# Kernel tuning notes

Hardware: AMD Instinct MI355X
Metric: run time of the kernel (lower is better)

Reference implementation:

```python
import jax, jax.numpy as jnp
import numpy as np

D = 1024        # input_dim
H = 4096        # hidden_dim (expert FFN width)
RH = H // 2     # router hidden
E = 8           # expert_count
TOP_K = 2
N = 4096        # tokens
LN_EPS = 1e-5


def setup_inputs() -> dict:
    key = jax.random.key(0)
    ks = jax.random.split(key, 12)
    s_d = 1.0 / np.sqrt(D)
    s_h = 1.0 / np.sqrt(H)
    s_rh = 1.0 / np.sqrt(RH)
    return {
        "x": jax.random.normal(ks[0], (N, D), jnp.float32),
        "ln_g": jnp.ones((D,), jnp.float32),
        "ln_b": jnp.zeros((D,), jnp.float32),
        # router: Linear(D, RH) -> ReLU -> Linear(RH, E)
        "rw1": jax.random.uniform(ks[1], (D, RH), jnp.float32, -s_d, s_d),
        "rb1": jax.random.uniform(ks[2], (RH,), jnp.float32, -s_d, s_d),
        "rw2": jax.random.uniform(ks[3], (RH, E), jnp.float32, -s_rh, s_rh),
        "rb2": jax.random.uniform(ks[4], (E,), jnp.float32, -s_rh, s_rh),
        # experts: E x (Linear(D, H) -> ReLU -> Linear(H, D)); dropout is identity in eval
        "ew1": jax.random.uniform(ks[5], (E, D, H), jnp.float32, -s_d, s_d),
        "eb1": jax.random.uniform(ks[6], (E, H), jnp.float32, -s_d, s_d),
        "ew2": jax.random.uniform(ks[7], (E, H, D), jnp.float32, -s_h, s_h),
        "eb2": jax.random.uniform(ks[8], (E, D), jnp.float32, -s_h, s_h),
    }


def reference(x, ln_g, ln_b, rw1, rb1, rw2, rb2, ew1, eb1, ew2, eb2):
    residual = x
    # LayerNorm
    mu = jnp.mean(x, axis=-1, keepdims=True)
    var = jnp.mean(jnp.square(x - mu), axis=-1, keepdims=True)
    xn = (x - mu) * jax.lax.rsqrt(var + LN_EPS) * ln_g + ln_b
    # Router MLP + softmax + top-k with renormalized gates
    logits = jax.nn.relu(xn @ rw1 + rb1) @ rw2 + rb2          # [N, E]
    probs = jax.nn.softmax(logits, axis=-1)
    vals, idx = jax.lax.top_k(probs, TOP_K)                    # [N, K]
    vals = vals / jnp.sum(vals, axis=-1, keepdims=True)
    # combine weights per expert: [N, E]
    combine = jnp.sum(jax.nn.one_hot(idx, E, dtype=vals.dtype) * vals[..., None], axis=1)
    # dense grouped expert FFN: h [E, N, H], y [E, N, D]
    h = jax.nn.relu(jnp.einsum("nd,edh->enh", xn, ew1) + eb1[:, None, :])
    y = jnp.einsum("enh,ehd->end", h, ew2) + eb2[:, None, :]
    out = residual + jnp.einsum("end,ne->nd", y, combine)
    return out
```

## Files before the change

kernel.cpp:

```cpp
#include <hip/hip_runtime.h>
#include <stdint.h>

#define D_    1024
#define H_    4096
#define RH_   2048
#define E_    8
#define N_    4096
#define NK_   8192
#define MT_MAX 71
#define DELTA_MARGIN 1e-4f
#define FIX_CAP 256

typedef __bf16 bf16x8 __attribute__((ext_vector_type(8)));
typedef float  f32x4  __attribute__((ext_vector_type(4)));


__device__ __forceinline__ unsigned short f2bf(float f) {
  union { float f; unsigned u; } v; v.f = f;
  unsigned r = v.u + 0x7fffu + ((v.u >> 16) & 1u);
  return (unsigned short)(r >> 16);
}
__device__ __forceinline__ float bf2f(unsigned short h) {
  union { unsigned u; float f; } v; v.u = ((unsigned)h) << 16;
  return v.f;
}

#define GLOAD16(gp, lp) \
  __builtin_amdgcn_global_load_lds((__attribute__((address_space(1))) void*)(void*)(gp), \
                                   (__attribute__((address_space(3))) void*)(lp), 16, 0, 0)

__global__ __launch_bounds__(256) void k_transpose(const float* __restrict__ in,
                                                   unsigned short* __restrict__ outH,
                                                   unsigned short* __restrict__ outL,
                                                   int R, int C) {
  __shared__ float t[64][65];
  const int b = blockIdx.z;
  const int c0 = blockIdx.x * 64, r0 = blockIdx.y * 64;
  const int lx = threadIdx.x & 63, ly = threadIdx.x >> 6;
  const long inB = (long)R * C;
  const float* ip = in + b * inB + (long)r0 * C + c0 + lx;
  #pragma unroll
  for (int i = 0; i < 16; i++)
    t[ly + i * 4][lx] = ip[(long)(ly + i * 4) * C];
  __syncthreads();
  const int wy = threadIdx.x >> 2;
  const int wx = (threadIdx.x & 3) * 16;
  const int c = c0 + wy;
  const long ob = b * inB + (long)c * R + r0 + wx;
  unsigned short h[16];
  #pragma unroll
  for (int j = 0; j < 16; j++) h[j] = f2bf(t[wx + j][wy]);
  #pragma unroll
  for (int j = 0; j < 4; j++)
    *(ushort4*)&outH[ob + j * 4] = make_ushort4(h[j*4], h[j*4+1], h[j*4+2], h[j*4+3]);
  if (outL) {
    unsigned short l[16];
    #pragma unroll
    for (int j = 0; j < 16; j++) l[j] = f2bf(t[wx + j][wy] - bf2f(h[j]));
    #pragma unroll
    for (int j = 0; j < 4; j++)
      *(ushort4*)&outL[ob + j * 4] = make_ushort4(l[j*4], l[j*4+1], l[j*4+2], l[j*4+3]);
  }
}

__global__ __launch_bounds__(256) void k_layernorm(const float* __restrict__ x,
                                                   const float* __restrict__ g,
                                                   const float* __restrict__ b,
                                                   unsigned short* __restrict__ xnh,
                                                   unsigned short* __restrict__ xnl) {
  __shared__ float red[4];
  const int n = blockIdx.x, tid = threadIdx.x;
  float4 v = ((const float4*)(x + (long)n * D_))[tid];
  float s = v.x + v.y + v.z + v.w;
  #pragma unroll
  for (int o = 32; o >= 1; o >>= 1) s += __shfl_xor(s, o, 64);
  if ((tid & 63) == 0) red[tid >> 6] = s;
  __syncthreads();
  float mean = (red[0] + red[1] + red[2] + red[3]) * (1.f / D_);
  __syncthreads();
  float d0 = v.x - mean, d1 = v.y - mean, d2 = v.z - mean, d3 = v.w - mean;
  float ss = d0 * d0 + d1 * d1 + d2 * d2 + d3 * d3;
  #pragma unroll
  for (int o = 32; o >= 1; o >>= 1) ss += __shfl_xor(ss, o, 64);
  if ((tid & 63) == 0) red[tid >> 6] = ss;
  __syncthreads();
  float rstd = rsqrtf((red[0] + red[1] + red[2] + red[3]) * (1.f / D_) + 1e-5f);
  float4 gg = ((const float4*)g)[tid];
  float4 bb = ((const float4*)b)[tid];
  float xn0 = d0 * rstd * gg.x + bb.x;
  float xn1 = d1 * rstd * gg.y + bb.y;
  float xn2 = d2 * rstd * gg.z + bb.z;
  float xn3 = d3 * rstd * gg.w + bb.w;
  unsigned short h0 = f2bf(xn0), h1 = f2bf(xn1), h2 = f2bf(xn2), h3 = f2bf(xn3);
  ((ushort4*)xnh)[(long)n * 256 + tid] = make_ushort4(h0, h1, h2, h3);
  ((ushort4*)xnl)[(long)n * 256 + tid] = make_ushort4(
      f2bf(xn0 - bf2f(h0)), f2bf(xn1 - bf2f(h1)),
      f2bf(xn2 - bf2f(h2)), f2bf(xn3 - bf2f(h3)));
}

__global__ void k_init(int* ctl) { if (threadIdx.x < 36) ctl[threadIdx.x] = 0; }

__global__ __launch_bounds__(256) void k_router_gemm(const unsigned short* __restrict__ xh,
                                                     const unsigned short* __restrict__ xl,
                                                     const unsigned short* __restrict__ bhT,
                                                     const unsigned short* __restrict__ blT,
                                                     const float* __restrict__ rb1,
                                                     float* __restrict__ h_r) {
  __shared__ __align__(16) unsigned short Ah[128 * 32], Al[128 * 32], Bh[128 * 32], Bl[128 * 32];
  const int tid = threadIdx.x, lane = tid & 63, wid = tid >> 6;
  const int m0 = blockIdx.x * 128, n0 = blockIdx.y * 128;
  const int wm = wid >> 1, wn = wid & 1;
  const int seg0 = wid * 2;
  const int srow = lane >> 2;
  const int scol = (lane & 3) * 8;
  const long a0 = (long)(m0 + seg0 * 16 + srow) * D_ + scol;
  const long a1 = a0 + 16 * D_;
  const long b0 = (long)(n0 + seg0 * 16 + srow) * D_ + scol;
  const long b1 = b0 + 16 * D_;
  const int rl = lane & 15, kh8 = (lane >> 4) * 8;
  f32x4 acc[4][4];
  #pragma unroll
  for (int i = 0; i < 4; i++)
    #pragma unroll
    for (int j = 0; j < 4; j++) acc[i][j] = 0.f;

  for (int k0 = 0; k0 < D_; k0 += 32) {
    GLOAD16(xh + a0 + k0, Ah + seg0 * 512);
    GLOAD16(xh + a1 + k0, Ah + seg0 * 512 + 512);
    GLOAD16(xl + a0 + k0, Al + seg0 * 512);
    GLOAD16(xl + a1 + k0, Al + seg0 * 512 + 512);
    GLOAD16(bhT + b0 + k0, Bh + seg0 * 512);
    GLOAD16(bhT + b1 + k0, Bh + seg0 * 512 + 512);
    GLOAD16(blT + b0 + k0, Bl + seg0 * 512);
    GLOAD16(blT + b1 + k0, Bl + seg0 * 512 + 512);
    __syncthreads();
    bf16x8 bhf[4], blf[4];
    #pragma unroll
    for (int ni = 0; ni < 4; ni++) {
      int r = (wn * 64 + ni * 16 + rl) * 32 + kh8;
      bhf[ni] = *(const bf16x8*)(Bh + r);
      blf[ni] = *(const bf16x8*)(Bl + r);
    }
    #pragma unroll
    for (int mi = 0; mi < 4; mi++) {
      int r = (wm * 64 + mi * 16 + rl) * 32 + kh8;
      bf16x8 ah = *(const bf16x8*)(Ah + r);
      bf16x8 al = *(const bf16x8*)(Al + r);
      #pragma unroll
      for (int ni = 0; ni < 4; ni++) {
        acc[mi][ni] = __builtin_amdgcn_mfma_f32_16x16x32_bf16(ah, bhf[ni], acc[mi][ni], 0, 0, 0);
        acc[mi][ni] = __builtin_amdgcn_mfma_f32_16x16x32_bf16(ah, blf[ni], acc[mi][ni], 0, 0, 0);
        acc[mi][ni] = __builtin_amdgcn_mfma_f32_16x16x32_bf16(al, bhf[ni], acc[mi][ni], 0, 0, 0);
      }
    }
    __syncthreads();
  }
  const int rg4 = (lane >> 4) * 4;
  #pragma unroll
  for (int ni = 0; ni < 4; ni++) {
    int col = n0 + wn * 64 + ni * 16 + rl;
    float bias = rb1[col];
    #pragma unroll
    for (int mi = 0; mi < 4; mi++) {
      int row = m0 + wm * 64 + mi * 16 + rg4;
      #pragma unroll
      for (int r = 0; r < 4; r++) {
        float v = acc[mi][ni][r] + bias;
        h_r[(long)(row + r) * RH_ + col] = v > 0.f ? v : 0.f;
      }
    }
  }
}

__global__ __launch_bounds__(256) void k_logits_top2(const float* __restrict__ h_r,
                                                     const float* __restrict__ rw2,
                                                     const float* __restrict__ rb2,
                                                     int* __restrict__ sel, float* __restrict__ gate,
                                                     int* __restrict__ marked, int* __restrict__ mcount) {
  const int lane = threadIdx.x & 63, wid = threadIdx.x >> 6;
  const int n = blockIdx.x * 4 + wid;
  float p[8] = {0, 0, 0, 0, 0, 0, 0, 0};
  const float* hr = h_r + (long)n * RH_;
  for (int i = 0; i < RH_ / 64; i++) {
    int c = i * 64 + lane;
    float v = hr[c];
    float4 wa = ((const float4*)(rw2 + c * 8))[0];
    float4 wb = ((const float4*)(rw2 + c * 8))[1];
    p[0] += v * wa.x; p[1] += v * wa.y; p[2] += v * wa.z; p[3] += v * wa.w;
    p[4] += v * wb.x; p[5] += v * wb.y; p[6] += v * wb.z; p[7] += v * wb.w;
  }
  #pragma unroll
  for (int e = 0; e < 8; e++)
    #pragma unroll
    for (int s = 32; s >= 1; s >>= 1) p[e] += __shfl_xor(p[e], s, 64);
  if (lane == 0) {
    float l1 = -1e30f, l2 = -1e30f, l3 = -1e30f; int e1 = 0, e2 = 0;
    #pragma unroll
    for (int e = 0; e < 8; e++) {
      float v = p[e] + rb2[e];
      if (v > l1)      { l3 = l2; l2 = l1; e2 = e1; l1 = v; e1 = e; }
      else if (v > l2) { l3 = l2; l2 = v; e2 = e; }
      else if (v > l3) { l3 = v; }
    }
    float g1 = 1.f / (1.f + expf(l2 - l1));
    sel[n * 2] = e1; sel[n * 2 + 1] = e2;
    gate[n * 2] = g1; gate[n * 2 + 1] = 1.f - g1;
    if (l2 - l3 < DELTA_MARGIN) { int i = atomicAdd(mcount, 1); marked[i] = n; }
  }
}

__global__ __launch_bounds__(256) void k_fixup1(const float* __restrict__ x,
                                                const float* __restrict__ ln_g, const float* __restrict__ ln_b,
                                                const float* __restrict__ rw1, const float* __restrict__ rb1,
                                                const int* __restrict__ marked, const int* __restrict__ mcount,
                                                double* __restrict__ hsbuf) {
  __shared__ float xs[D_];
  __shared__ float redf[4];
  __shared__ double part[64][5];
  const int tid = threadIdx.x;
  int cnt = *mcount; if (cnt > FIX_CAP) cnt = FIX_CAP;
  const int blkTok = blockIdx.x >> 5;
  const int chunk  = blockIdx.x & 31;
  for (int mi = blkTok; mi < cnt; mi += FIX_CAP) {
    const int n = marked[mi];
    float4 v = ((const float4*)(x + (long)n * D_))[tid];
    float s = v.x + v.y + v.z + v.w;
    #pragma unroll
    for (int o = 32; o >= 1; o >>= 1) s += __shfl_xor(s, o, 64);
    if ((tid & 63) == 0) redf[tid >> 6] = s;
    __syncthreads();
    float mean = (redf[0] + redf[1] + redf[2] + redf[3]) * (1.f / D_);
    __syncthreads();
    float d0 = v.x - mean, d1 = v.y - mean, d2 = v.z - mean, d3 = v.w - mean;
    float ss = d0 * d0 + d1 * d1 + d2 * d2 + d3 * d3;
    #pragma unroll
    for (int o = 32; o >= 1; o >>= 1) ss += __shfl_xor(ss, o, 64);
    if ((tid & 63) == 0) redf[tid >> 6] = ss;
    __syncthreads();
    float rstd = rsqrtf((redf[0] + redf[1] + redf[2] + redf[3]) * (1.f / D_) + 1e-5f);
    float4 gg = ((const float4*)ln_g)[tid];
    float4 bb = ((const float4*)ln_b)[tid];
    xs[tid * 4 + 0] = d0 * rstd * gg.x + bb.x;
    xs[tid * 4 + 1] = d1 * rstd * gg.y + bb.y;
    xs[tid * 4 + 2] = d2 * rstd * gg.z + bb.z;
    xs[tid * 4 + 3] = d3 * rstd * gg.w + bb.w;
    __syncthreads();
    const int lcol = tid & 63, prt = tid >> 6;
    const int col = chunk * 64 + lcol;
    const float* rp = rw1 + (long)(prt * 256) * RH_ + col;
    const float* xp = xs + prt * 256;
    double a0 = 0, a1 = 0, a2 = 0, a3 = 0;
    #pragma unroll 4
    for (int d = 0; d < 256; d += 4) {
      float w0 = rp[(long)(d + 0) * RH_];
      float w1 = rp[(long)(d + 1) * RH_];
      float w2 = rp[(long)(d + 2) * RH_];
      float w3 = rp[(long)(d + 3) * RH_];
      a0 += (double)xp[d + 0] * (double)w0;
      a1 += (double)xp[d + 1] * (double)w1;
      a2 += (double)xp[d + 2] * (double)w2;
      a3 += (double)xp[d + 3] * (double)w3;
    }
    part[lcol][prt] = (a0 + a1) + (a2 + a3);
    __syncthreads();
    if (tid < 64) {
      double a = (part[tid][0] + part[tid][1]) + (part[tid][2] + part[tid][3])
               + (double)rb1[chunk * 64 + tid];
      hsbuf[(long)mi * RH_ + chunk * 64 + tid] = a > 0.0 ? a : 0.0;
    }
    __syncthreads();
  }
}

__global__ __launch_bounds__(256) void k_fixup2(const double* __restrict__ hsbuf,
                                                const float* __restrict__ rw2, const float* __restrict__ rb2,
                                                const int* __restrict__ marked, const int* __restrict__ mcount,
                                                int* __restrict__ sel, float* __restrict__ gate) {
  __shared__ double red2[256];
  const int tid = threadIdx.x;
  int cnt = *mcount; if (cnt > FIX_CAP) cnt = FIX_CAP;
  for (int mi = blockIdx.x; mi < cnt; mi += gridDim.x) {
    const int n = marked[mi];
    const double* hs = hsbuf + (long)mi * RH_;
    const int e = tid & 7, ch = tid >> 3;
    double pp = 0.0;
    for (int c = ch * 64; c < ch * 64 + 64; c++) pp += hs[c] * (double)rw2[c * 8 + e];
    red2[tid] = pp;
    __syncthreads();
    if (tid < 128) red2[tid] += red2[tid + 128];
    __syncthreads();
    if (tid < 64) red2[tid] += red2[tid + 64];
    __syncthreads();
    if (tid < 32) red2[tid] += red2[tid + 32];
    __syncthreads();
    if (tid < 16) red2[tid] += red2[tid + 16];
    __syncthreads();
    if (tid < 8) red2[tid] += red2[tid + 8];
    __syncthreads();
    if (tid == 0) {
      double l1 = -1e300, l2 = -1e300; int e1 = 0, e2 = 0;
      for (int ee = 0; ee < 8; ee++) {
        double vv = red2[ee] + (double)rb2[ee];
        if (vv > l1)      { l2 = l1; e2 = e1; l1 = vv; e1 = ee; }
        else if (vv > l2) { l2 = vv; e2 = ee; }
      }
      double g1 = 1.0 / (1.0 + exp(l2 - l1));
      sel[n * 2] = e1; sel[n * 2 + 1] = e2;
      gate[n * 2] = (float)g1; gate[n * 2 + 1] = (float)(1.0 - g1);
    }
    __syncthreads();
  }
}

__global__ void k_count(const int* __restrict__ sel, int* ctl) {
  int n = blockIdx.x * 256 + threadIdx.x;
  if (n >= N_) return;
  atomicAdd(&ctl[sel[n * 2]], 1);
  atomicAdd(&ctl[sel[n * 2 + 1]], 1);
}
__global__ void k_offsets(int* ctl) {
  if (threadIdx.x == 0 && blockIdx.x == 0) {
    int t = 0, tt = 0;
    for (int e = 0; e < 8; e++) {
      ctl[8 + e] = t; ctl[17 + e] = tt; ctl[26 + e] = t;
      t += ctl[e]; tt += (ctl[e] + 127) >> 7;
    }
    ctl[16] = t; ctl[25] = tt;
  }
}
__global__ void k_scatter(const int* __restrict__ sel, int* ctl,
                          int* __restrict__ perm, int* __restrict__ pos) {
  int n = blockIdx.x * 256 + threadIdx.x;
  if (n >= N_) return;
  #pragma unroll
  for (int k = 0; k < 2; k++) {
    int e = sel[n * 2 + k];
    int p = atomicAdd(&ctl[26 + e], 1);
    perm[p] = n;
    pos[n * 2 + k] = p;
  }
}

template <int KD, bool GATHER, bool RELU_BF16, bool MTFAST>
__global__ __launch_bounds__(256) void k_gemm_expert5(const unsigned short* __restrict__ A,
                                                      const unsigned short* __restrict__ BT,
                                                      const float* __restrict__ bias,
                                                      const int* __restrict__ ctl,
                                                      const int* __restrict__ perm,
                                                      unsigned short* __restrict__ outBF,
                                                      float* __restrict__ outF32, int NB) {
  const int* cnt = ctl; const int* off = ctl + 8; const int* toff = ctl + 17;
  const int NX = gridDim.x, MT = gridDim.y;
  const int nwg = NX * MT;
  const int F = blockIdx.y * NX + blockIdx.x;
  const int q = nwg >> 3, r8 = nwg & 7;
  const int xcd = F & 7, j = F >> 3;
  const int L = (xcd < r8 ? xcd * (q + 1) : r8 * (q + 1) + (xcd - r8) * q) + j;
  int mt, nt;
  if (MTFAST) { mt = L % MT; nt = L / MT; }
  else        { nt = L % NX; mt = L / NX; }
  if (mt >= toff[8]) return;
  int e = 0;
  #pragma unroll
  for (int i = 0; i < 7; i++) if (toff[i + 1] <= mt) e = i + 1;
  const int ltile = mt - toff[e];
  const int g0 = off[e] + ltile * 128;
  int vrows = cnt[e] - ltile * 128; if (vrows > 128) vrows = 128;
  const int n0 = nt * 128;

  __shared__ __align__(16) unsigned short At[2][128 * 64];
  __shared__ __align__(16) unsigned short Bt[2][128 * 64];
  const int tid = threadIdx.x, lane = tid & 63, wid = tid >> 6;
  const int l8 = lane >> 3, s8 = lane & 7;
  const int ksw = (s8 ^ l8) * 8;

  long aa[4], bb[4];
  const long bbase = (long)e * NB * KD;
  const int gmax = off[e] + cnt[e] - 1;
  #pragma unroll
  for (int i = 0; i < 4; i++) {
    int row = wid * 32 + i * 8 + l8;
    long ar;
    if constexpr (GATHER) {
      int g = g0 + row;
      ar = perm[g <= gmax ? g : gmax];
    } else {
      ar = g0 + row;
    }
    aa[i] = ar * (long)KD + ksw;
    bb[i] = bbase + (long)(n0 + row) * KD + ksw;
  }

  const int wm = wid >> 1, wn = wid & 1;
  const int rl = lane & 15, g4 = lane >> 4;
  int sA[2];
  #pragma unroll
  for (int kk = 0; kk < 2; kk++)
    sA[kk] = ((kk * 4 + g4) ^ (rl & 7)) * 8;

  f32x4 acc[4][4];
  #pragma unroll
  for (int i = 0; i < 4; i++)
    #pragma unroll
    for (int jj = 0; jj < 4; jj++) acc[i][jj] = 0.f;

  auto stage = [&](int bi, int k0) {
    #pragma unroll
    for (int i = 0; i < 4; i++) {
      GLOAD16(A + aa[i] + k0, &At[bi][(wid * 32 + i * 8) * 64]);
      GLOAD16(BT + bb[i] + k0, &Bt[bi][(wid * 32 + i * 8) * 64]);
    }
  };
  auto compute = [&](int bi) {
    #pragma unroll
    for (int kk = 0; kk < 2; kk++) {
      bf16x8 bfr[4];
      #pragma unroll
      for (int ni = 0; ni < 4; ni++)
        bfr[ni] = *(const bf16x8*)(&Bt[bi][(wn * 64 + ni * 16 + rl) * 64 + sA[kk]]);
      #pragma unroll
      for (int mi = 0; mi < 4; mi++) {
        bf16x8 af = *(const bf16x8*)(&At[bi][(wm * 64 + mi * 16 + rl) * 64 + sA[kk]]);
        #pragma unroll
        for (int ni = 0; ni < 4; ni++)
          acc[mi][ni] = __builtin_amdgcn_mfma_f32_16x16x32_bf16(af, bfr[ni], acc[mi][ni], 0, 0, 0);
      }
    }
  };

  constexpr int NT = KD / 64;
  stage(0, 0);
  stage(1, 64);
  int cur = 0;
  #pragma unroll 1
  for (int t = 0; t < NT - 2; ++t) {
    asm volatile("s_waitcnt vmcnt(8)" ::: "memory");
    __builtin_amdgcn_sched_barrier(0);
    __builtin_amdgcn_s_barrier();
    asm volatile("" ::: "memory");
    compute(cur);
    asm volatile("" ::: "memory");
    __builtin_amdgcn_s_barrier();
    stage(cur, (t + 2) * 64);
    cur ^= 1;
  }
  asm volatile("s_waitcnt vmcnt(8)" ::: "memory");
  __builtin_amdgcn_sched_barrier(0);
  __builtin_amdgcn_s_barrier();
  asm volatile("" ::: "memory");
  compute(cur);
  asm volatile("" ::: "memory");
  __builtin_amdgcn_s_barrier();
  cur ^= 1;
  asm volatile("s_waitcnt vmcnt(0)" ::: "memory");
  __builtin_amdgcn_sched_barrier(0);
  __builtin_amdgcn_s_barrier();
  asm volatile("" ::: "memory");
  compute(cur);

  const int rg4 = (lane >> 4) * 4;
  #pragma unroll
  for (int ni = 0; ni < 4; ni++) {
    int col = n0 + wn * 64 + ni * 16 + rl;
    float bv = bias[(long)e * NB + col];
    #pragma unroll
    for (int mi = 0; mi < 4; mi++) {
      int lrow = wm * 64 + mi * 16 + rg4;
      #pragma unroll
      for (int r = 0; r < 4; r++) {
        if (lrow + r < vrows) {
          float v = acc[mi][ni][r] + bv;
          long idx = (long)(g0 + lrow + r) * NB + col;
          if constexpr (RELU_BF16) outBF[idx] = f2bf(v > 0.f ? v : 0.f);
          else outF32[idx] = v;
        }
      }
    }
  }
}

__global__ __launch_bounds__(256) void k_combine(const float* __restrict__ x,
                                                 const float* __restrict__ y_buf,
                                                 const int* __restrict__ pos,
                                                 const float* __restrict__ gate,
                                                 float* __restrict__ out) {
  const int n = blockIdx.x, t = threadIdx.x;
  const float g0 = gate[n * 2], g1 = gate[n * 2 + 1];
  const long p0 = pos[n * 2], p1 = pos[n * 2 + 1];
  float4 xv = ((const float4*)(x + (long)n * D_))[t];
  float4 a = ((const float4*)(y_buf + p0 * D_))[t];
  float4 b = ((const float4*)(y_buf + p1 * D_))[t];
  float4 o;
  o.x = xv.x + g0 * a.x + g1 * b.x;
  o.y = xv.y + g0 * a.y + g1 * b.y;
  o.z = xv.z + g0 * a.z + g1 * b.z;
  o.w = xv.w + g0 * a.w + g1 * b.w;
  ((float4*)(out + (long)n * D_))[t] = o;
}

extern "C" void kernel_launch(void* const* d_in, const int* in_sizes, int n_in,
                              void* d_out, int out_size, void* d_ws, size_t ws_size,
                              hipStream_t stream) {
  const float* x    = (const float*)d_in[0];
  const float* ln_g = (const float*)d_in[1];
  const float* ln_b = (const float*)d_in[2];
  const float* rw1  = (const float*)d_in[3];
  const float* rb1  = (const float*)d_in[4];
  const float* rw2  = (const float*)d_in[5];
  const float* rb2  = (const float*)d_in[6];
  const float* ew1  = (const float*)d_in[7];
  const float* eb1  = (const float*)d_in[8];
  const float* ew2  = (const float*)d_in[9];
  const float* eb2  = (const float*)d_in[10];
  float* out = (float*)d_out;

  char* w = (char*)d_ws;
  size_t off = 0;
  auto alloc = [&](size_t bytes) -> char* {
    char* p = w + off;
    off += (bytes + 255) & ~(size_t)255;
    return p;
  };
  unsigned short* ew1T  = (unsigned short*)alloc((size_t)E_ * H_ * D_ * 2);
  unsigned short* ew2T  = (unsigned short*)alloc((size_t)E_ * D_ * H_ * 2);
  unsigned short* rw1hT = (unsigned short*)alloc((size_t)RH_ * D_ * 2);
  unsigned short* rw1lT = (unsigned short*)alloc((size_t)RH_ * D_ * 2);
  unsigned short* xnh   = (unsigned short*)alloc((size_t)N_ * D_ * 2);
  unsigned short* xnl   = (unsigned short*)alloc((size_t)N_ * D_ * 2);
  float*          h_r   = (float*)alloc((size_t)N_ * RH_ * 4);
  unsigned short* h_buf = (unsigned short*)alloc((size_t)(NK_ + 128) * H_ * 2);
  float*          y_buf = (float*)alloc((size_t)(NK_ + 128) * D_ * 4);
  double*         hsbuf = (double*)alloc((size_t)FIX_CAP * RH_ * 8);
  int*   sel    = (int*)alloc((size_t)N_ * 2 * 4);
  float* gate   = (float*)alloc((size_t)N_ * 2 * 4);
  int*   marked = (int*)alloc((size_t)N_ * 4);
  int*   perm   = (int*)alloc((size_t)NK_ * 4);
  int*   pos    = (int*)alloc((size_t)N_ * 2 * 4);
  int*   ctl    = (int*)alloc(64 * 4);

  k_transpose<<<dim3(H_ / 64, D_ / 64, E_), 256, 0, stream>>>(ew1, ew1T, nullptr, D_, H_);
  k_transpose<<<dim3(D_ / 64, H_ / 64, E_), 256, 0, stream>>>(ew2, ew2T, nullptr, H_, D_);
  k_transpose<<<dim3(RH_ / 64, D_ / 64, 1), 256, 0, stream>>>(rw1, rw1hT, rw1lT, D_, RH_);
  k_layernorm<<<N_, 256, 0, stream>>>(x, ln_g, ln_b, xnh, xnl);
  k_init<<<1, 64, 0, stream>>>(ctl);
  k_router_gemm<<<dim3(N_ / 128, RH_ / 128), 256, 0, stream>>>(xnh, xnl, rw1hT, rw1lT, rb1, h_r);
  k_logits_top2<<<N_ / 4, 256, 0, stream>>>(h_r, rw2, rb2, sel, gate, marked, ctl + 34);
  k_fixup1<<<FIX_CAP * 32, 256, 0, stream>>>(x, ln_g, ln_b, rw1, rb1, marked, ctl + 34, hsbuf);
  k_fixup2<<<64, 256, 0, stream>>>(hsbuf, rw2, rb2, marked, ctl + 34, sel, gate);
  k_count<<<N_ / 256, 256, 0, stream>>>(sel, ctl);
  k_offsets<<<1, 1, 0, stream>>>(ctl);
  k_scatter<<<N_ / 256, 256, 0, stream>>>(sel, ctl, perm, pos);
  k_gemm_expert5<D_, true, true, true><<<dim3(H_ / 128, MT_MAX), 256, 0, stream>>>(
      xnh, ew1T, eb1, ctl, perm, h_buf, nullptr, H_);
  k_gemm_expert5<H_, false, false, false><<<dim3(D_ / 128, MT_MAX), 256, 0, stream>>>(
      h_buf, ew2T, eb2, ctl, perm, nullptr, y_buf, D_);
  k_combine<<<N_, 256, 0, stream>>>(x, y_buf, pos, gate, out);

  (void)in_sizes; (void)n_in; (void)out_size; (void)ws_size;
}
```

Measured before the change: 584.6 us.

## Use 256x256 expert GEMM tiles with 8 waves and split-K second GEMM

Expert GEMMs move from 128x128 tiles with 4 waves to 256x256 tiles with 8 waves (512 threads). Loads are staged in four quarter-steps interleaved with MFMA sub-blocks under a raised s_setprio. This raises data reuse per tile and overlaps global loads with compute. The down-projection is split along K into two partial fp32 buffers, which the combine kernel sums, to recover parallelism lost to the larger tiles. In exchange it adds extra partial-output traffic, more padding waste per expert, and higher LDS and register pressure.

Measured after the change: 698.1 us. 19.4% more time.

```diff
diff --git a/kernel.cpp b/kernel.cpp
--- a/kernel.cpp
+++ b/kernel.cpp
@@ -8,8 +8,10 @@
 #define N_    4096
 #define NK_   8192
 #define MT_MAX 71
+#define MT256_MAX 39
 #define DELTA_MARGIN 1e-4f
 #define FIX_CAP 256
+#define PSTRIDE ((long)(NK_ + 256) * D_)
 
 typedef __bf16 bf16x8 __attribute__((ext_vector_type(8)));
 typedef float  f32x4  __attribute__((ext_vector_type(4)));
@@ -98,7 +100,7 @@
       f2bf(xn2 - bf2f(h2)), f2bf(xn3 - bf2f(h3)));
 }
 
-__global__ void k_init(int* ctl) { if (threadIdx.x < 36) ctl[threadIdx.x] = 0; }
+__global__ void k_init(int* ctl) { if (threadIdx.x < 46) ctl[threadIdx.x] = 0; }
 
 __global__ __launch_bounds__(256) void k_router_gemm(const unsigned short* __restrict__ xh,
                                                      const unsigned short* __restrict__ xl,
@@ -320,12 +322,12 @@
 }
 __global__ void k_offsets(int* ctl) {
   if (threadIdx.x == 0 && blockIdx.x == 0) {
-    int t = 0, tt = 0;
+    int t = 0, tt = 0, t2 = 0;
     for (int e = 0; e < 8; e++) {
-      ctl[8 + e] = t; ctl[17 + e] = tt; ctl[26 + e] = t;
-      t += ctl[e]; tt += (ctl[e] + 127) >> 7;
-    }
-    ctl[16] = t; ctl[25] = tt;
+      ctl[8 + e] = t; ctl[17 + e] = tt; ctl[26 + e] = t; ctl[36 + e] = t2;
+      t += ctl[e]; tt += (ctl[e] + 127) >> 7; t2 += (ctl[e] + 255) >> 8;
+    }
+    ctl[16] = t; ctl[25] = tt; ctl[44] = t2;
   }
 }
 __global__ void k_scatter(const int* __restrict__ sel, int* ctl,
@@ -341,15 +343,15 @@
   }
 }
 
-template <int KD, bool GATHER, bool RELU_BF16, bool MTFAST>
-__global__ __launch_bounds__(256) void k_gemm_expert5(const unsigned short* __restrict__ A,
-                                                      const unsigned short* __restrict__ BT,
-                                                      const float* __restrict__ bias,
-                                                      const int* __restrict__ ctl,
-                                                      const int* __restrict__ perm,
-                                                      unsigned short* __restrict__ outBF,
-                                                      float* __restrict__ outF32, int NB) {
-  const int* cnt = ctl; const int* off = ctl + 8; const int* toff = ctl + 17;
+template <int KD, int KB, bool GATHER, bool RELU_BF16, bool MTFAST>
+__global__ __launch_bounds__(512, 2) void k_gemm_expert8(const unsigned short* __restrict__ A,
+                                                         const unsigned short* __restrict__ BT,
+                                                         const float* __restrict__ bias,
+                                                         const int* __restrict__ ctl,
+                                                         const int* __restrict__ perm,
+                                                         unsigned short* __restrict__ outBF,
+                                                         float* __restrict__ outF32, int NB) {
+  const int* cnt = ctl; const int* off = ctl + 8; const int* toff = ctl + 36;
   const int NX = gridDim.x, MT = gridDim.y;
   const int nwg = NX * MT;
   const int F = blockIdx.y * NX + blockIdx.x;
@@ -364,22 +366,23 @@
   #pragma unroll
   for (int i = 0; i < 7; i++) if (toff[i + 1] <= mt) e = i + 1;
   const int ltile = mt - toff[e];
-  const int g0 = off[e] + ltile * 128;
-  int vrows = cnt[e] - ltile * 128; if (vrows > 128) vrows = 128;
-  const int n0 = nt * 128;
-
-  __shared__ __align__(16) unsigned short At[2][128 * 64];
-  __shared__ __align__(16) unsigned short Bt[2][128 * 64];
+  const int g0 = off[e] + ltile * 256;
+  int vrows = cnt[e] - ltile * 256; if (vrows > 256) vrows = 256;
+  const int n0 = nt * 256;
+  const long kbase = (long)blockIdx.z * KB;
+
+  __shared__ __align__(16) unsigned short At[2][256 * 64];
+  __shared__ __align__(16) unsigned short Bt[2][256 * 64];
   const int tid = threadIdx.x, lane = tid & 63, wid = tid >> 6;
   const int l8 = lane >> 3, s8 = lane & 7;
   const int ksw = (s8 ^ l8) * 8;
 
-  long aa[4], bb[4];
+  long aA[4], aB[4];
   const long bbase = (long)e * NB * KD;
   const int gmax = off[e] + cnt[e] - 1;
   #pragma unroll
   for (int i = 0; i < 4; i++) {
-    int row = wid * 32 + i * 8 + l8;
+    int row = i * 64 + wid * 8 + l8;
     long ar;
     if constexpr (GATHER) {
       int g = g0 + row;
@@ -387,92 +390,105 @@
     } else {
       ar = g0 + row;
     }
-    aa[i] = ar * (long)KD + ksw;
-    bb[i] = bbase + (long)(n0 + row) * KD + ksw;
-  }
-
-  const int wm = wid >> 1, wn = wid & 1;
+    aA[i] = ar * (long)KD + ksw + kbase;
+    aB[i] = bbase + (long)(n0 + row) * KD + ksw + kbase;
+  }
+
+  const int wm = wid >> 2, wn = wid & 3;
   const int rl = lane & 15, g4 = lane >> 4;
-  int sA[2];
-  #pragma unroll
-  for (int kk = 0; kk < 2; kk++)
-    sA[kk] = ((kk * 4 + g4) ^ (rl & 7)) * 8;
-
-  f32x4 acc[4][4];
-  #pragma unroll
-  for (int i = 0; i < 4; i++)
+  int sl[2];
+  #pragma unroll
+  for (int ks = 0; ks < 2; ks++) sl[ks] = ((ks * 4 + g4) ^ (rl & 7)) * 8;
+
+  f32x4 acc[8][4];
+  #pragma unroll
+  for (int i = 0; i < 8; i++)
     #pragma unroll
     for (int jj = 0; jj < 4; jj++) acc[i][jj] = 0.f;
 
-  auto stage = [&](int bi, int k0) {
-    #pragma unroll
-    for (int i = 0; i < 4; i++) {
-      GLOAD16(A + aa[i] + k0, &At[bi][(wid * 32 + i * 8) * 64]);
-      GLOAD16(BT + bb[i] + k0, &Bt[bi][(wid * 32 + i * 8) * 64]);
+  auto stage_ht = [&](int bi, int s, int k0) {
+    if (s < 2) {
+      #pragma unroll
+      for (int i = 0; i < 2; i++) {
+        int is = s * 2 + i;
+        GLOAD16(A + aA[is] + k0, &At[bi][(is * 64 + wid * 8) * 64]);
+      }
+    } else {
+      #pragma unroll
+      for (int i = 0; i < 2; i++) {
+        int is = (s - 2) * 2 + i;
+        GLOAD16(BT + aB[is] + k0, &Bt[bi][(is * 64 + wid * 8) * 64]);
+      }
     }
   };
-  auto compute = [&](int bi) {
-    #pragma unroll
-    for (int kk = 0; kk < 2; kk++) {
-      bf16x8 bfr[4];
-      #pragma unroll
-      for (int ni = 0; ni < 4; ni++)
-        bfr[ni] = *(const bf16x8*)(&Bt[bi][(wn * 64 + ni * 16 + rl) * 64 + sA[kk]]);
-      #pragma unroll
-      for (int mi = 0; mi < 4; mi++) {
-        bf16x8 af = *(const bf16x8*)(&At[bi][(wm * 64 + mi * 16 + rl) * 64 + sA[kk]]);
-        #pragma unroll
-        for (int ni = 0; ni < 4; ni++)
-          acc[mi][ni] = __builtin_amdgcn_mfma_f32_16x16x32_bf16(af, bfr[ni], acc[mi][ni], 0, 0, 0);
-      }
-    }
-  };
-
-  constexpr int NT = KD / 64;
-  stage(0, 0);
-  stage(1, 64);
+
+  constexpr int NT = KB / 64;
+  #pragma unroll
+  for (int s = 0; s < 4; s++) stage_ht(0, s, 0);
+
   int cur = 0;
   #pragma unroll 1
-  for (int t = 0; t < NT - 2; ++t) {
-    asm volatile("s_waitcnt vmcnt(8)" ::: "memory");
-    __builtin_amdgcn_sched_barrier(0);
-    __builtin_amdgcn_s_barrier();
-    asm volatile("" ::: "memory");
-    compute(cur);
-    asm volatile("" ::: "memory");
-    __builtin_amdgcn_s_barrier();
-    stage(cur, (t + 2) * 64);
+  for (int t = 0; t < NT; ++t) {
+    const int k1 = (t + 1) * 64;
+    #pragma unroll
+    for (int p = 0; p < 4; ++p) {
+      const int qm = p >> 1, qn = p & 1;
+      if (p == 0) {
+        if (t + 1 < NT) {
+          stage_ht(cur ^ 1, 0, k1);
+          asm volatile("s_waitcnt vmcnt(2)" ::: "memory");
+        } else {
+          asm volatile("s_waitcnt vmcnt(0)" ::: "memory");
+        }
+        __builtin_amdgcn_sched_barrier(0);
+        __builtin_amdgcn_s_barrier();
+        asm volatile("" ::: "memory");
+      } else {
+        if (t + 1 < NT) stage_ht(cur ^ 1, p, k1);
+      }
+      __builtin_amdgcn_s_setprio(1);
+      bf16x8 bfr[2][2];
+      #pragma unroll
+      for (int ni = 0; ni < 2; ni++)
+        #pragma unroll
+        for (int ks = 0; ks < 2; ks++)
+          bfr[ni][ks] = *(const bf16x8*)&Bt[cur][(wn * 64 + (qn * 2 + ni) * 16 + rl) * 64 + sl[ks]];
+      #pragma unroll
+      for (int mi = 0; mi < 4; mi++) {
+        const int arow = (wm * 128 + (qm * 4 + mi) * 16 + rl) * 64;
+        bf16x8 a0 = *(const bf16x8*)&At[cur][arow + sl[0]];
+        bf16x8 a1 = *(const bf16x8*)&At[cur][arow + sl[1]];
+        #pragma unroll
+        for (int ni = 0; ni < 2; ni++) {
+          acc[qm * 4 + mi][qn * 2 + ni] =
+              __builtin_amdgcn_mfma_f32_16x16x32_bf16(a0, bfr[ni][0], acc[qm * 4 + mi][qn * 2 + ni], 0, 0, 0);
+          acc[qm * 4 + mi][qn * 2 + ni] =
+              __builtin_amdgcn_mfma_f32_16x16x32_bf16(a1, bfr[ni][1], acc[qm * 4 + mi][qn * 2 + ni], 0, 0, 0);
+        }
+      }
+      __builtin_amdgcn_s_setprio(0);
+      __builtin_amdgcn_s_barrier();
+      asm volatile("" ::: "memory");
+    }
     cur ^= 1;
   }
-  asm volatile("s_waitcnt vmcnt(8)" ::: "memory");
-  __builtin_amdgcn_sched_barrier(0);
-  __builtin_amdgcn_s_barrier();
-  asm volatile("" ::: "memory");
-  compute(cur);
-  asm volatile("" ::: "memory");
-  __builtin_amdgcn_s_barrier();
-  cur ^= 1;
-  asm volatile("s_waitcnt vmcnt(0)" ::: "memory");
-  __builtin_amdgcn_sched_barrier(0);
-  __builtin_amdgcn_s_barrier();
-  asm volatile("" ::: "memory");
-  compute(cur);
-
+
+  float* outZ = outF32 ? outF32 + (long)blockIdx.z * PSTRIDE : nullptr;
   const int rg4 = (lane >> 4) * 4;
   #pragma unroll
   for (int ni = 0; ni < 4; ni++) {
     int col = n0 + wn * 64 + ni * 16 + rl;
-    float bv = bias[(long)e * NB + col];
-    #pragma unroll
-    for (int mi = 0; mi < 4; mi++) {
-      int lrow = wm * 64 + mi * 16 + rg4;
+    float bv = (blockIdx.z == 0) ? bias[(long)e * NB + col] : 0.f;
+    #pragma unroll
+    for (int mi = 0; mi < 8; mi++) {
+      int lrow = wm * 128 + mi * 16 + rg4;
       #pragma unroll
       for (int r = 0; r < 4; r++) {
         if (lrow + r < vrows) {
           float v = acc[mi][ni][r] + bv;
           long idx = (long)(g0 + lrow + r) * NB + col;
           if constexpr (RELU_BF16) outBF[idx] = f2bf(v > 0.f ? v : 0.f);
-          else outF32[idx] = v;
+          else outZ[idx] = v;
         }
       }
     }
@@ -480,7 +496,7 @@
 }
 
 __global__ __launch_bounds__(256) void k_combine(const float* __restrict__ x,
-                                                 const float* __restrict__ y_buf,
+                                                 const float* __restrict__ y_part,
                                                  const int* __restrict__ pos,
                                                  const float* __restrict__ gate,
                                                  float* __restrict__ out) {
@@ -488,13 +504,15 @@
   const float g0 = gate[n * 2], g1 = gate[n * 2 + 1];
   const long p0 = pos[n * 2], p1 = pos[n * 2 + 1];
   float4 xv = ((const float4*)(x + (long)n * D_))[t];
-  float4 a = ((const float4*)(y_buf + p0 * D_))[t];
-  float4 b = ((const float4*)(y_buf + p1 * D_))[t];
+  float4 a0 = ((const float4*)(y_part + p0 * D_))[t];
+  float4 a1 = ((const float4*)(y_part + PSTRIDE + p0 * D_))[t];
+  float4 b0 = ((const float4*)(y_part + p1 * D_))[t];
+  float4 b1 = ((const float4*)(y_part + PSTRIDE + p1 * D_))[t];
   float4 o;
-  o.x = xv.x + g0 * a.x + g1 * b.x;
-  o.y = xv.y + g0 * a.y + g1 * b.y;
-  o.z = xv.z + g0 * a.z + g1 * b.z;
-  o.w = xv.w + g0 * a.w + g1 * b.w;
+  o.x = xv.x + g0 * (a0.x + a1.x) + g1 * (b0.x + b1.x);
+  o.y = xv.y + g0 * (a0.y + a1.y) + g1 * (b0.y + b1.y);
+  o.z = xv.z + g0 * (a0.z + a1.z) + g1 * (b0.z + b1.z);
+  o.w = xv.w + g0 * (a0.w + a1.w) + g1 * (b0.w + b1.w);
   ((float4*)(out + (long)n * D_))[t] = o;
 }
 
@@ -528,8 +546,8 @@
   unsigned short* xnh   = (unsigned short*)alloc((size_t)N_ * D_ * 2);
   unsigned short* xnl   = (unsigned short*)alloc((size_t)N_ * D_ * 2);
   float*          h_r   = (float*)alloc((size_t)N_ * RH_ * 4);
-  unsigned short* h_buf = (unsigned short*)alloc((size_t)(NK_ + 128) * H_ * 2);
-  float*          y_buf = (float*)alloc((size_t)(NK_ + 128) * D_ * 4);
+  unsigned short* h_buf = (unsigned short*)alloc((size_t)(NK_ + 256) * H_ * 2);
+  float*          y_part = (float*)alloc((size_t)2 * PSTRIDE * 4);
   double*         hsbuf = (double*)alloc((size_t)FIX_CAP * RH_ * 8);
   int*   sel    = (int*)alloc((size_t)N_ * 2 * 4);
   float* gate   = (float*)alloc((size_t)N_ * 2 * 4);
@@ -550,11 +568,11 @@
   k_count<<<N_ / 256, 256, 0, stream>>>(sel, ctl);
   k_offsets<<<1, 1, 0, stream>>>(ctl);
   k_scatter<<<N_ / 256, 256, 0, stream>>>(sel, ctl, perm, pos);
-  k_gemm_expert5<D_, true, true, true><<<dim3(H_ / 128, MT_MAX), 256, 0, stream>>>(
+  k_gemm_expert8<D_, D_, true, true, true><<<dim3(H_ / 256, MT256_MAX, 1), 512, 0, stream>>>(
       xnh, ew1T, eb1, ctl, perm, h_buf, nullptr, H_);
-  k_gemm_expert5<H_, false, false, false><<<dim3(D_ / 128, MT_MAX), 256, 0, stream>>>(
-      h_buf, ew2T, eb2, ctl, perm, nullptr, y_buf, D_);
-  k_combine<<<N_, 256, 0, stream>>>(x, y_buf, pos, gate, out);
+  k_gemm_expert8<H_, H_ / 2, false, false, false><<<dim3(D_ / 256, MT256_MAX, 2), 512, 0, stream>>>(
+      h_buf, ew2T, eb2, ctl, perm, nullptr, y_part, D_);
+  k_combine<<<N_, 256, 0, stream>>>(x, y_part, pos, gate, out);
 
   (void)in_sizes; (void)n_in; (void)out_size; (void)ws_size;
 }
```
